# Performance work log

Hardware: AMD Instinct MI355X
Metric: run time of the kernel (lower is better)

Reference implementation:

```python
import jax, jax.numpy as jnp
import numpy as np

N = 50000      # nodes
E = 800000     # edges
D_IN = 128
D_H = 512
D_OUT = 256
G = 512        # graphs in batch
EPS_GIN = 0.0  # GINConv default eps
LRELU_SLOPE = 1.5


def setup_inputs() -> dict:
    key = jax.random.key(0)
    ks = jax.random.split(key, 16)
    x = jax.random.normal(ks[0], (N, D_IN), dtype=jnp.float32)
    edge_index = jax.random.randint(ks[1], (2, E), 0, N, dtype=jnp.int64)
    batch = jnp.sort(jax.random.randint(ks[2], (N,), 0, G, dtype=jnp.int64))
    def lin(k, fan_in, fan_out):
        bound = 1.0 / np.sqrt(fan_in)
        k1, k2 = jax.random.split(k)
        W = jax.random.uniform(k1, (fan_in, fan_out), jnp.float32, -bound, bound)
        b = jax.random.uniform(k2, (fan_out,), jnp.float32, -bound, bound)
        return W, b
    W1, b1 = lin(ks[3], D_IN, D_H)
    W2, b2 = lin(ks[4], D_H, D_H)
    W3, b3 = lin(ks[5], D_H, D_H)
    W4, b4 = lin(ks[6], D_H, D_H)
    Wl, bl = lin(ks[7], D_H, D_OUT)
    return {"x": x, "edge_index": edge_index, "batch": batch,
            "W1": W1, "b1": b1, "W2": W2, "b2": b2,
            "W3": W3, "b3": b3, "W4": W4, "b4": b4,
            "Wl": Wl, "bl": bl}


def reference(x, edge_index, batch, W1, b1, W2, b2, W3, b3, W4, b4, Wl, bl):
    # GIN aggregation: sum neighbor (source) features at each target node
    src, dst = edge_index[0], edge_index[1]
    agg = jax.ops.segment_sum(x[src], dst, num_segments=N)  # [N, D_IN]
    h = (1.0 + EPS_GIN) * x + agg
    # 4-layer MLP (Dropout inactive in eval; LeakyReLU negative_slope=1.5)
    h = h @ W1 + b1
    h = jnp.where(h > 0, h, LRELU_SLOPE * h)
    h = jax.nn.relu(h @ W2 + b2)
    h = jax.nn.relu(h @ W3 + b3)
    h = h @ W4 + b4                      # [N, D_H]
    # global mean pool over graphs
    sums = jax.ops.segment_sum(h, batch, num_segments=G)          # [G, D_H]
    cnt = jax.ops.segment_sum(jnp.ones((N, 1), h.dtype), batch, num_segments=G)
    pooled = sums / jnp.maximum(cnt, 1.0)
    out = pooled @ Wl + bl               # [G, D_OUT]
    # F.normalize(dim=1, eps=1e-12)
    nrm = jnp.linalg.norm(out, axis=1, keepdims=True)
    return out / jnp.maximum(nrm, 1e-12)
```

## Files before the change

### kernel.cpp

```cpp
#include <hip/hip_runtime.h>
#include <hip/hip_bf16.h>
#include <cstdint>
#include <cstddef>

#define N_NODES 50000
#define N_EDGES 800000
#define D_IN 128
#define D_H 512
#define D_OUT 256
#define N_GRAPHS 512

#define BM 128
#define BN 256
#define BK 32
#define NBLK ((N_NODES + 255) / 256)
#define CT_SW 264
#define N_MT 391
#define MT_PER_XCD 49

#define NBUCK 196
#define BCAP 6144
#define E_PER_BLK 4096

#define SCAT_BLKS 196
#define TR_BLKS 240
#define CVTX_BLKS ((N_NODES * D_IN / 2 + 64 + 255) / 256)
#define MID_BLKS (SCAT_BLKS + TR_BLKS + CVTX_BLKS)

#define WC_BLKS 64

#define PSLOTS 5

#define XQ_SCALE 4096.0f
#define XQ_INV (1.0f / 4096.0f)

typedef __bf16 v8bf __attribute__((ext_vector_type(8)));
typedef float v4f __attribute__((ext_vector_type(4)));
typedef int v4i __attribute__((ext_vector_type(4)));

__device__ __forceinline__ float bf2f(unsigned short b) {
  return __uint_as_float(((unsigned int)b) << 16);
}
__device__ __forceinline__ unsigned short f2bf(float f) {
  unsigned int u = __float_as_uint(f);
  u += 0x7FFFu + ((u >> 16) & 1u);
  return (unsigned short)(u >> 16);
}

__device__ __forceinline__ void gload_lds16(const void* g, void* l) {
  __builtin_amdgcn_global_load_lds(
      (const __attribute__((address_space(1))) void*)g,
      (__attribute__((address_space(3))) void*)l, 16, 0, 0);
}

__global__ __launch_bounds__(256) void k_prep(const void* __restrict__ x,
                                              const void* __restrict__ ei,
                                              const void* __restrict__ batch,
                                              int* __restrict__ gcur,
                                              int* __restrict__ flags) {
  __shared__ int cnt[3];
  int t = threadIdx.x;
  gcur[t] = 0;
  if (t < 3) cnt[t] = 0;
  __syncthreads();
  const unsigned short* xs = (const unsigned short*)x;
  int c0 = 0;
  for (int k = t; k < 4096; k += 256) {
    unsigned int e = (xs[k] >> 7) & 0xFFu;
    if (e >= 0x90u) c0++;
  }
  atomicAdd(&cnt[0], c0);
  const int* e32 = (const int*)ei;
  int c1 = 0;
  for (int k = t; k < 512; k += 256)
    if (e32[2 * k + 1] != 0) c1++;
  atomicAdd(&cnt[1], c1);
  const int* b32 = (const int*)batch;
  int c2 = 0;
  {
    int w = (N_NODES - 512) + 2 * t + 1;
    if (b32[w] != 0) c2++;
  }
  atomicAdd(&cnt[2], c2);
  __syncthreads();
  if (t == 0) {
    flags[0] = (cnt[0] > 16) ? 1 : 0;
    flags[1] = (cnt[1] == 0) ? 1 : 0;
    flags[2] = (cnt[2] == 0) ? 1 : 0;
  }
}

__global__ __launch_bounds__(256) void k_mid(
    const void* __restrict__ x, const int* __restrict__ ei,
    const int* __restrict__ flags,
    const void* W1, const void* W2, const void* W3, const void* W4,
    const void* Wl, unsigned short* W1T, unsigned short* W2T,
    unsigned short* W3T, unsigned short* W4T, unsigned short* WlT,
    int* __restrict__ gcur, unsigned int* __restrict__ pairs,
    unsigned int* __restrict__ xi, int ne) {
  __shared__ __align__(16) char mshm[20480];
  int bid = blockIdx.x;
  int t = threadIdx.x;

  if (bid < SCAT_BLKS) {
    int* hist = (int*)mshm;
    int* sstart = hist + 256;
    int* gbase = sstart + 256;
    int* sh = gbase + 256;
    unsigned int* lbuf = (unsigned int*)(mshm + 4096);
    int e0 = bid * E_PER_BLK;
    int nloc = ne - e0;
    if (nloc > E_PER_BLK) nloc = E_PER_BLK;
    hist[t] = 0;
    __syncthreads();
    bool fe64 = flags[1] != 0;
    unsigned int pk[16];
    short bk[16], rk[16];
#pragma unroll
    for (int it = 0; it < 16; ++it) {
      int li = it * 256 + t;
      bk[it] = -1;
      if (li < nloc) {
        size_t e = (size_t)e0 + li;
        int s = fe64 ? ei[2 * e] : ei[e];
        int d = fe64 ? ei[2 * ((size_t)ne + e)] : ei[(size_t)ne + e];
        int b = d >> 8;
        pk[it] = (unsigned int)(s & 0xFFFF) | ((unsigned int)(d & 255) << 16) |
                 ((unsigned int)b << 24);
        bk[it] = (short)b;
        rk[it] = (short)atomicAdd(&hist[b], 1);
      }
    }
    __syncthreads();
    int cnt = hist[t];
    sh[t] = cnt;
    __syncthreads();
    for (int o = 1; o < 256; o <<= 1) {
      int a = sh[t];
      int bb = (t >= o) ? sh[t - o] : 0;
      __syncthreads();
      sh[t] = a + bb;
      __syncthreads();
    }
    sstart[t] = sh[t] - cnt;
    gbase[t] = (cnt > 0) ? atomicAdd(&gcur[t], cnt) : 0;
    __syncthreads();
#pragma unroll
    for (int it = 0; it < 16; ++it)
      if (bk[it] >= 0) lbuf[sstart[bk[it]] + rk[it]] = pk[it];
    __syncthreads();
    for (int i = t; i < nloc; i += 256) {
      unsigned int v = lbuf[i];
      int b = v >> 24;
      int off = gbase[b] + (i - sstart[b]);
      if (off < BCAP) pairs[(size_t)b * BCAP + off] = v;
    }
    return;
  }

  if (bid < SCAT_BLKS + TR_BLKS) {
    typedef unsigned short row65[65];
    row65* tile = (row65*)mshm;
    int b2 = bid - SCAT_BLKS;
    const void* src;
    unsigned short* dst;
    int R, C, tb;
    if (b2 < 16)        { src = W1; dst = W1T; R = 128; C = 512; tb = b2; }
    else if (b2 < 80)   { src = W2; dst = W2T; R = 512; C = 512; tb = b2 - 16; }
    else if (b2 < 144)  { src = W3; dst = W3T; R = 512; C = 512; tb = b2 - 80; }
    else if (b2 < 208)  { src = W4; dst = W4T; R = 512; C = 512; tb = b2 - 144; }
    else                { src = Wl; dst = WlT; R = 512; C = 256; tb = b2 - 208; }
    int tpr = C >> 6;
    int r0 = (tb / tpr) << 6, c0 = (tb % tpr) << 6;
    bool f32 = flags[0] != 0;
#pragma unroll
    for (int k = 0; k < 16; ++k) {
      int idx = k * 256 + t;
      int r = idx >> 6, c = idx & 63;
      unsigned short v =
          f32 ? f2bf(((const float*)src)[(size_t)(r0 + r) * C + c0 + c])
              : ((const unsigned short*)src)[(size_t)(r0 + r) * C + c0 + c];
      tile[c][r] = v;
    }
    __syncthreads();
#pragma unroll
    for (int k = 0; k < 16; ++k) {
      int idx = k * 256 + t;
      int r = idx >> 6, c = idx & 63;
      dst[(size_t)(c0 + r) * R + r0 + c] = tile[r][c];
    }
    return;
  }

  int i = (bid - SCAT_BLKS - TR_BLKS) * 256 + t;
  if (i >= N_NODES * D_IN / 2) {
    if (i < N_NODES * D_IN / 2 + 64) xi[i] = 0;
    return;
  }
  float v0, v1;
  if (flags[0]) {
    const float* xf = (const float*)x + (size_t)i * 2;
    v0 = xf[0];
    v1 = xf[1];
  } else {
    unsigned int p = ((const unsigned int*)x)[i];
    v0 = __uint_as_float((p & 0xFFFFu) << 16);
    v1 = __uint_as_float(p & 0xFFFF0000u);
  }
  int q0 = __float2int_rn(fminf(fmaxf(v0, -7.99f), 7.99f) * XQ_SCALE);
  int q1 = __float2int_rn(fminf(fmaxf(v1, -7.99f), 7.99f) * XQ_SCALE);
  xi[i] = ((unsigned int)q0 & 0xFFFFu) | ((unsigned int)q1 << 16);
}

__global__ __launch_bounds__(256) void kb_sort(
    const unsigned int* __restrict__ pairs, const int* __restrict__ gcur,
    int* __restrict__ rowptr, unsigned short* __restrict__ elist,
    const unsigned short* __restrict__ W4T,
    const unsigned short* __restrict__ WlT,
    const void* __restrict__ b4, const void* __restrict__ bl,
    const int* __restrict__ flags,
    unsigned short* __restrict__ WcT, float* __restrict__ bc) {
  __shared__ int sh[256];
  __shared__ int cursor[256];
  __shared__ unsigned int lpair[BCAP];
  __shared__ unsigned short sorted[BCAP];
  int b = blockIdx.x, t = threadIdx.x;

  if (b >= NBUCK) {
    int wb = b - NBUCK;
    if (wb < WC_BLKS) {
      float (*wlt)[4] = (float(*)[4])lpair;
      int n0w = wb * 4;
      for (int e = t; e < 2048; e += 256) {
        int j = e >> 2, ns = e & 3;
        wlt[j][ns] = bf2f(WlT[(size_t)(n0w + ns) * 512 + j]);
      }
      __syncthreads();
      float a0[4] = {0.f, 0.f, 0.f, 0.f}, a1[4] = {0.f, 0.f, 0.f, 0.f};
      for (int j = 0; j < 512; ++j) {
        v4f wv = *(const v4f*)&wlt[j][0];
        float x0 = bf2f(W4T[(size_t)j * 512 + t]);
        float x1 = bf2f(W4T[(size_t)j * 512 + t + 256]);
#pragma unroll
        for (int q = 0; q < 4; ++q) {
          a0[q] += x0 * wv[q];
          a1[q] += x1 * wv[q];
        }
      }
#pragma unroll
      for (int q = 0; q < 4; ++q) {
        WcT[(size_t)(n0w + q) * 512 + t]       = f2bf(a0[q]);
        WcT[(size_t)(n0w + q) * 512 + t + 256] = f2bf(a1[q]);
      }
    } else {
      float* bsh = (float*)lpair;
      bool fmw = flags[0] != 0;
      for (int e = t; e < 512; e += 256)
        bsh[e] = fmw ? ((const float*)b4)[e]
                     : bf2f(((const unsigned short*)b4)[e]);
      __syncthreads();
      float a = fmw ? ((const float*)bl)[t]
                    : bf2f(((const unsigned short*)bl)[t]);
      for (int j = 0; j < 512; ++j)
        a += bsh[j] * bf2f(WlT[(size_t)t * 512 + j]);
      bc[t] = a;
    }
    return;
  }

  int c = (t < NBUCK) ? gcur[t] : 0;
  if (c > BCAP) c = BCAP;
  sh[t] = c;
  __syncthreads();
  for (int o = 1; o < 256; o <<= 1) {
    int a = sh[t];
    int v = (t >= o) ? sh[t - o] : 0;
    __syncthreads();
    sh[t] = a + v;
    __syncthreads();
  }
  int base = (b == 0) ? 0 : sh[b - 1];
  int cnt = sh[b] - base;
  cursor[t] = 0;
  __syncthreads();
  for (int i = t; i < cnt; i += 256) {
    unsigned int v = pairs[(size_t)b * BCAP + i];
    lpair[i] = v;
    atomicAdd(&cursor[(v >> 16) & 255], 1);
  }
  __syncthreads();
  int nc = cursor[t];
  sh[t] = nc;
  __syncthreads();
  for (int o = 1; o < 256; o <<= 1) {
    int a = sh[t];
    int v = (t >= o) ? sh[t - o] : 0;
    __syncthreads();
    sh[t] = a + v;
    __syncthreads();
  }
  int nstart = sh[t] - nc;
  cursor[t] = nstart;
  int node = b * 256 + t;
  if (node <= N_NODES) rowptr[node] = base + nstart;
  __syncthreads();
  for (int i = t; i < cnt; i += 256) {
    unsigned int v = lpair[i];
    int r = atomicAdd(&cursor[(v >> 16) & 255], 1);
    sorted[r] = (unsigned short)(v & 0xFFFFu);
  }
  __syncthreads();
  for (int i = t; i < cnt; i += 256)
    elist[base + i] = sorted[i];
}

__global__ __launch_bounds__(256) void k_gather(
    const unsigned int* __restrict__ xi, const int* __restrict__ rowptr,
    const unsigned short* __restrict__ elist, unsigned int* __restrict__ h0) {
  int node = blockIdx.x * 4 + (threadIdx.x >> 6);
  if (node >= N_NODES) return;
  int lane = threadIdx.x & 63;
  int l15 = lane & 15;
  int grp = lane >> 4;
  int s0 = rowptr[node], s1 = rowptr[node + 1];
  int a[8];
  {
    v4i self = (v4i){0, 0, 0, 0};
    if (lane < 16) self = *(const v4i*)(xi + (size_t)node * 64 + l15 * 4);
#pragma unroll
    for (int q = 0; q < 4; ++q) {
      a[2 * q]     = (int)(short)(self[q] & 0xFFFF);
      a[2 * q + 1] = self[q] >> 16;
    }
  }
  for (int j0 = s0; j0 < s1; j0 += 64) {
    int jj = j0 + lane;
    int cnt = s1 - j0;
    cnt = cnt < 64 ? cnt : 64;
    int ev = (jj < s1) ? (int)elist[jj] : N_NODES;
    for (int j = 0; j < cnt; j += 4) {
      int src = __shfl(ev, j + grp, 64);
      v4i p = *(const v4i*)(xi + (size_t)src * 64 + l15 * 4);
#pragma unroll
      for (int q = 0; q < 4; ++q) {
        a[2 * q]     += (int)(short)(p[q] & 0xFFFF);
        a[2 * q + 1] += p[q] >> 16;
      }
    }
  }
#pragma unroll
  for (int k = 0; k < 8; ++k) {
    a[k] += __shfl_xor(a[k], 16, 64);
    a[k] += __shfl_xor(a[k], 32, 64);
  }
  if (lane < 16) {
    v4i o;
#pragma unroll
    for (int q = 0; q < 4; ++q) {
      unsigned int lo = f2bf((float)a[2 * q] * XQ_INV);
      unsigned int hi = f2bf((float)a[2 * q + 1] * XQ_INV);
      o[q] = (int)(lo | (hi << 16));
    }
    *(v4i*)(h0 + (size_t)node * 64 + l15 * 4) = o;
  }
}

template <int ACT, int OUT, bool SWZ, bool FB = false>
__global__ __launch_bounds__(512, 4) void gemm_bt(
    const unsigned short* __restrict__ A,
    const unsigned short* __restrict__ BT,
    const void* __restrict__ bias, const int* __restrict__ flags,
    const int* __restrict__ batchp, void* __restrict__ Cout,
    int M, int K, int Nc) {
  __shared__ __align__(16) unsigned short smem[2][BM * BK + BN * BK];

  const int tid  = threadIdx.x;
  const int wave = tid >> 6;
  const int lane = tid & 63;
  const int quad = lane >> 4;
  const int l15  = lane & 15;
  int m0, n0;
  if (SWZ) {
    int xcd = blockIdx.x & 7;
    int l = blockIdx.x >> 3;
    int mt = xcd * MT_PER_XCD + (l >> 1);
    if (mt >= N_MT) return;
    m0 = mt * BM;
    n0 = (l & 1) * BN;
  } else {
    n0 = blockIdx.x * BN;
    m0 = blockIdx.y * BM;
  }
  const int wm = (wave >> 2) * 64;
  const int wn = (wave & 3) * 64;
  const bool fm = flags[0] != 0;

  v4f acc[4][4];
#pragma unroll
  for (int i = 0; i < 4; ++i)
#pragma unroll
    for (int j = 0; j < 4; ++j) acc[i][j] = (v4f){0.f, 0.f, 0.f, 0.f};

  auto stage = [&](int kt, int buf) {
    const int k0 = kt * BK;
    unsigned short* As = smem[buf];
    unsigned short* Bs = smem[buf] + BM * BK;
    {
      int L = tid;
      int row = L >> 2;
      int c = (L & 3) ^ ((row >> 1) & 3);
      int gr = m0 + row;
      gr = gr < M ? gr : (M - 1);
      gload_lds16(A + (size_t)gr * K + (k0 + c * 8), As + (size_t)L * 8);
    }
#pragma unroll
    for (int it = 0; it < 2; ++it) {
      int L = tid + it * 512;
      int row = L >> 2;
      int c = (L & 3) ^ ((row >> 1) & 3);
      int gn = n0 + row;
      gload_lds16(BT + (size_t)gn * K + (k0 + c * 8), Bs + (size_t)L * 8);
    }
  };

  const int nK = K / BK;
  stage(0, 0);
  for (int kt = 0; kt < nK; ++kt) {
    __syncthreads();
    if (kt + 1 < nK) stage(kt + 1, (kt + 1) & 1);
    const unsigned short* As = smem[kt & 1];
    const unsigned short* Bs = smem[kt & 1] + BM * BK;
    v8bf af[4], bfr[4];
#pragma unroll
    for (int mi = 0; mi < 4; ++mi) {
      int r = wm + mi * 16 + l15;
      int s = quad ^ ((r >> 1) & 3);
      af[mi] = *(const v8bf*)(As + (r * 4 + s) * 8);
    }
#pragma unroll
    for (int ni = 0; ni < 4; ++ni) {
      int r = wn + ni * 16 + l15;
      int s = quad ^ ((r >> 1) & 3);
      bfr[ni] = *(const v8bf*)(Bs + (r * 4 + s) * 8);
    }
#pragma unroll
    for (int mi = 0; mi < 4; ++mi)
#pragma unroll
      for (int ni = 0; ni < 4; ++ni)
        acc[mi][ni] = __builtin_amdgcn_mfma_f32_16x16x32_bf16(
            af[mi], bfr[ni], acc[mi][ni], 0, 0, 0);
  }

  float bv[4];
#pragma unroll
  for (int ni = 0; ni < 4; ++ni) {
    int col = n0 + wn + ni * 16 + l15;
    bv[ni] = (fm || FB) ? ((const float*)bias)[col]
                        : bf2f(((const unsigned short*)bias)[col]);
  }
#pragma unroll
  for (int mi = 0; mi < 4; ++mi)
#pragma unroll
    for (int ni = 0; ni < 4; ++ni)
#pragma unroll
      for (int rg = 0; rg < 4; ++rg) {
        float v = acc[mi][ni][rg] + bv[ni];
        if (ACT == 0) v = v > 0.f ? v : 1.5f * v;
        if (ACT == 1) v = v > 0.f ? v : 0.f;
        acc[mi][ni][rg] = v;
      }

  if (OUT == 1) {
#pragma unroll
    for (int ni = 0; ni < 4; ++ni) {
      int col = n0 + wn + ni * 16 + l15;
#pragma unroll
      for (int mi = 0; mi < 4; ++mi)
#pragma unroll
        for (int rg = 0; rg < 4; ++rg) {
          int row = m0 + wm + mi * 16 + quad * 4 + rg;
          if (row < M)
            ((float*)Cout)[(size_t)row * Nc + col] = acc[mi][ni][rg];
        }
    }
    return;
  }

  if (OUT == 2) {
    float* ssq = (float*)smem;
    __syncthreads();
    float pp[4][4];
#pragma unroll
    for (int mi = 0; mi < 4; ++mi)
#pragma unroll
      for (int rg = 0; rg < 4; ++rg) {
        float s = 0.f;
#pragma unroll
        for (int ni = 0; ni < 4; ++ni) {
          float v = acc[mi][ni][rg];
          s += v * v;
        }
#pragma unroll
        for (int o = 1; o < 16; o <<= 1) s += __shfl_xor(s, o, 64);
        pp[mi][rg] = s;
      }
    if (l15 == 0) {
#pragma unroll
      for (int mi = 0; mi < 4; ++mi)
#pragma unroll
        for (int rg = 0; rg < 4; ++rg)
          ssq[(wave & 3) * 128 + wm + mi * 16 + quad * 4 + rg] = pp[mi][rg];
    }
    __syncthreads();
#pragma unroll
    for (int mi = 0; mi < 4; ++mi)
#pragma unroll
      for (int rg = 0; rg < 4; ++rg) {
        int row = wm + mi * 16 + quad * 4 + rg;
        float tot = (ssq[row] + ssq[128 + row]) + (ssq[256 + row] + ssq[384 + row]);
        float inv = 1.0f / fmaxf(sqrtf(tot), 1e-12f);
        int grow = m0 + row;
#pragma unroll
        for (int ni = 0; ni < 4; ++ni) {
          int col = wn + ni * 16 + l15;
          float r = acc[mi][ni][rg] * inv;
          if (fm)
            ((float*)Cout)[(size_t)grow * Nc + col] = r;
          else
            ((unsigned short*)Cout)[(size_t)grow * Nc + col] = f2bf(r);
        }
      }
    return;
  }

  if (OUT == 3) {
    float* part = (float*)smem;
    __syncthreads();
    for (int i = tid; i < 8 * PSLOTS * 256; i += 512) part[i] = 0.f;
    const int contrib = (wave >> 2) * 4 + quad;
    const bool b64 = flags[2] != 0;
    int g0 = b64 ? batchp[2 * (size_t)m0] : batchp[m0];
    __syncthreads();
    int curslot = -1;
    float r0 = 0.f, r1 = 0.f, r2 = 0.f, r3 = 0.f;
#pragma unroll
    for (int mi = 0; mi < 4; ++mi)
#pragma unroll
      for (int rg = 0; rg < 4; ++rg) {
        int grow = m0 + wm + mi * 16 + quad * 4 + rg;
        if (grow < M) {
          int gv = (b64 ? batchp[2 * (size_t)grow] : batchp[grow]) - g0;
          gv = gv < 0 ? 0 : (gv >= PSLOTS ? PSLOTS - 1 : gv);
          if (gv != curslot) {
            if (curslot >= 0) {
              float* pp = part + (contrib * PSLOTS + curslot) * 256 + wn + l15;
              pp[0] += r0; pp[16] += r1; pp[32] += r2; pp[48] += r3;
            }
            curslot = gv;
            r0 = r1 = r2 = r3 = 0.f;
          }
          r0 += acc[mi][0][rg];
          r1 += acc[mi][1][rg];
          r2 += acc[mi][2][rg];
          r3 += acc[mi][3][rg];
        }
      }
    if (curslot >= 0) {
      float* pp = part + (contrib * PSLOTS + curslot) * 256 + wn + l15;
      pp[0] += r0; pp[16] += r1; pp[32] += r2; pp[48] += r3;
    }
    __syncthreads();
    float* pb = (float*)Cout;
    int mt = m0 >> 7;
    int nh = n0 >> 8;
    size_t base = (size_t)(mt * 2 + nh) * (PSLOTS * 256);
    for (int i = tid; i < PSLOTS * 256; i += 512) {
      float s = ((part[i] + part[1 * PSLOTS * 256 + i]) +
                 (part[2 * PSLOTS * 256 + i] + part[3 * PSLOTS * 256 + i])) +
                ((part[4 * PSLOTS * 256 + i] + part[5 * PSLOTS * 256 + i]) +
                 (part[6 * PSLOTS * 256 + i] + part[7 * PSLOTS * 256 + i]));
      pb[base + i] = s;
    }
    return;
  }

  unsigned short* Ct = (unsigned short*)smem;
  __syncthreads();
#pragma unroll
  for (int h = 0; h < 2; ++h) {
    if ((wave >> 2) == h) {
#pragma unroll
      for (int mi = 0; mi < 4; ++mi)
#pragma unroll
        for (int ni = 0; ni < 4; ++ni)
#pragma unroll
          for (int rg = 0; rg < 4; ++rg) {
            int lr = mi * 16 + quad * 4 + rg;
            int c = wn + ni * 16 + l15;
            Ct[lr * CT_SW + c] = f2bf(acc[mi][ni][rg]);
          }
    }
    __syncthreads();
    int rl0 = tid >> 5;
    int ch = tid & 31;
#pragma unroll
    for (int p = 0; p < 4; ++p) {
      int rl = rl0 + p * 16;
      int grow = m0 + h * 64 + rl;
      if (grow < M) {
        v4i val = *(const v4i*)(Ct + rl * CT_SW + ch * 8);
        *(v4i*)((unsigned short*)Cout + (size_t)grow * Nc + n0 + ch * 8) = val;
      }
    }
    __syncthreads();
  }
}

__global__ __launch_bounds__(256) void k_cvtpool(
    const float* __restrict__ pb, const int* __restrict__ batch,
    const int* __restrict__ flags, unsigned int* __restrict__ pooled) {
  __shared__ int bounds[2];
  int g = blockIdx.x, t = threadIdx.x;
  bool b64 = flags[2] != 0;
  if (t < 2) {
    int key = g + t;
    int lo = 0, hi = N_NODES;
    while (lo < hi) {
      int mid = (lo + hi) >> 1;
      int bv = b64 ? batch[2 * (size_t)mid] : batch[mid];
      if (bv < key) lo = mid + 1; else hi = mid;
    }
    bounds[t] = lo;
  }
  __syncthreads();
  int s0 = bounds[0], s1 = bounds[1];
  int c0 = 2 * t;
  int nh = c0 >> 8;
  int cl = c0 & 255;
  float a0 = 0.f, a1 = 0.f;
  if (s1 > s0) {
    int mtlo = s0 >> 7, mthi = (s1 - 1) >> 7;
    for (int mt = mtlo; mt <= mthi; ++mt) {
      int g0 = b64 ? batch[2 * (size_t)(mt * 128)] : batch[mt * 128];
      int slot = g - g0;
      if (slot >= 0 && slot < PSLOTS) {
        size_t base = (size_t)(mt * 2 + nh) * (PSLOTS * 256) + (size_t)slot * 256;
        a0 += pb[base + cl];
        a1 += pb[base + cl + 1];
      }
    }
  }
  float inv = 1.0f / fmaxf((float)(s1 - s0), 1.0f);
  unsigned int lo2 = f2bf(a0 * inv);
  unsigned int hi2 = f2bf(a1 * inv);
  pooled[(size_t)g * (D_H / 2) + t] = lo2 | (hi2 << 16);
}

extern "C" void kernel_launch(void* const* d_in, const int* in_sizes, int n_in,
                              void* d_out, int out_size, void* d_ws,
                              size_t ws_size, hipStream_t stream) {
  const void* x    = d_in[0];
  const int* ei    = (const int*)d_in[1];
  const int* batch = (const int*)d_in[2];
  const void* W1 = d_in[3];
  const void* b1 = d_in[4];
  const void* W2 = d_in[5];
  const void* b2 = d_in[6];
  const void* W3 = d_in[7];
  const void* b3 = d_in[8];
  const void* W4 = d_in[9];
  const void* b4 = d_in[10];
  const void* Wl = d_in[11];
  const void* bl = d_in[12];

  char* ws = (char*)d_ws;
  size_t off = 0;
  auto alloc = [&](size_t bytes) {
    void* p = ws + off;
    off += (bytes + 255) & ~(size_t)255;
    return p;
  };
  int* flags           = (int*)alloc(64);
  unsigned short* W1T  = (unsigned short*)alloc((size_t)D_IN * D_H * 2);
  unsigned short* W2T  = (unsigned short*)alloc((size_t)D_H * D_H * 2);
  unsigned short* W3T  = (unsigned short*)alloc((size_t)D_H * D_H * 2);
  unsigned short* W4T  = (unsigned short*)alloc((size_t)D_H * D_H * 2);
  unsigned short* WlT  = (unsigned short*)alloc((size_t)D_H * D_OUT * 2);
  unsigned short* WcT  = (unsigned short*)alloc((size_t)D_OUT * D_H * 2);
  float* bc            = (float*)alloc((size_t)D_OUT * 4);
  unsigned int* pooled3 = (unsigned int*)alloc((size_t)N_GRAPHS * D_H * 2);
  float* pb            = (float*)alloc((size_t)N_MT * 2 * PSLOTS * 256 * 4);
  int* gcur   = (int*)alloc(256 * 4);
  int* rowptr = (int*)alloc(((size_t)N_NODES + 1) * 4);
  unsigned short* elist = (unsigned short*)alloc((size_t)N_EDGES * 2);
  void* S1 = alloc((size_t)N_NODES * D_H * 2);
  void* S2 = alloc((size_t)N_NODES * D_H * 2);
  unsigned int* xi   = (unsigned int*)S1;
  unsigned short* hA = (unsigned short*)S1;
  unsigned int* pairs = (unsigned int*)((char*)S1 + ((size_t)16 << 20));
  unsigned int* h0u  = (unsigned int*)S2;
  unsigned short* h0 = (unsigned short*)S2;
  unsigned short* hB = (unsigned short*)S2;

  k_prep<<<1, 256, 0, stream>>>(x, ei, batch, gcur, flags);

  k_mid<<<MID_BLKS, 256, 0, stream>>>(
      x, ei, flags, W1, W2, W3, W4, Wl, W1T, W2T, W3T, W4T, WlT,
      gcur, pairs, xi, N_EDGES);

  kb_sort<<<NBUCK + WC_BLKS + 1, 256, 0, stream>>>(
      pairs, gcur, rowptr, elist, W4T, WlT, b4, bl, flags, WcT, bc);
  k_gather<<<(N_NODES + 3) / 4, 256, 0, stream>>>(xi, rowptr, elist, h0u);

  const int gBig = 8 * MT_PER_XCD * 2;
  gemm_bt<0, 0, true><<<gBig, 512, 0, stream>>>(
      h0, W1T, b1, flags, batch, hA, N_NODES, D_IN, D_H);
  gemm_bt<1, 0, true><<<gBig, 512, 0, stream>>>(
      hA, W2T, b2, flags, batch, hB, N_NODES, D_H, D_H);
  gemm_bt<1, 3, true><<<gBig, 512, 0, stream>>>(
      hB, W3T, b3, flags, batch, pb, N_NODES, D_H, D_H);

  k_cvtpool<<<N_GRAPHS, 256, 0, stream>>>(pb, batch, flags, pooled3);

  dim3 g5(1, 4);
  gemm_bt<2, 2, false, true><<<g5, 512, 0, stream>>>(
      (const unsigned short*)pooled3, WcT, bc, flags, batch, d_out,
      N_GRAPHS, D_H, D_OUT);
}
```

Measured before the change: 290.4 us.

## Fold format-detection prep kernel into k_mid and unroll gather loop by two

Removes the single-block k_prep launch by having every k_mid block recompute the dtype-detection counts it needs locally, with block 0 writing the flags for later kernels, and replaces gcur zeroing with a memset. This drops one serialized kernel launch and its dependency. Separately, the neighbor gather loop now issues two row loads per iteration to raise memory-level parallelism. Every k_mid block redundantly reads a few KB of input, and the 8-stride loop relies on padded elist entries pointing to a zeroed row.

```diff
diff --git a/kernel.cpp b/kernel.cpp
--- a/kernel.cpp
+++ b/kernel.cpp
@@ -53,56 +53,47 @@
       (__attribute__((address_space(3))) void*)l, 16, 0, 0);
 }
 
-__global__ __launch_bounds__(256) void k_prep(const void* __restrict__ x,
-                                              const void* __restrict__ ei,
-                                              const void* __restrict__ batch,
-                                              int* __restrict__ gcur,
-                                              int* __restrict__ flags) {
-  __shared__ int cnt[3];
-  int t = threadIdx.x;
-  gcur[t] = 0;
-  if (t < 3) cnt[t] = 0;
-  __syncthreads();
-  const unsigned short* xs = (const unsigned short*)x;
-  int c0 = 0;
-  for (int k = t; k < 4096; k += 256) {
-    unsigned int e = (xs[k] >> 7) & 0xFFu;
-    if (e >= 0x90u) c0++;
-  }
-  atomicAdd(&cnt[0], c0);
-  const int* e32 = (const int*)ei;
-  int c1 = 0;
-  for (int k = t; k < 512; k += 256)
-    if (e32[2 * k + 1] != 0) c1++;
-  atomicAdd(&cnt[1], c1);
-  const int* b32 = (const int*)batch;
-  int c2 = 0;
-  {
-    int w = (N_NODES - 512) + 2 * t + 1;
-    if (b32[w] != 0) c2++;
-  }
-  atomicAdd(&cnt[2], c2);
-  __syncthreads();
-  if (t == 0) {
-    flags[0] = (cnt[0] > 16) ? 1 : 0;
-    flags[1] = (cnt[1] == 0) ? 1 : 0;
-    flags[2] = (cnt[2] == 0) ? 1 : 0;
-  }
-}
-
 __global__ __launch_bounds__(256) void k_mid(
     const void* __restrict__ x, const int* __restrict__ ei,
-    const int* __restrict__ flags,
+    const void* __restrict__ batch, int* __restrict__ flagsOut,
     const void* W1, const void* W2, const void* W3, const void* W4,
     const void* Wl, unsigned short* W1T, unsigned short* W2T,
     unsigned short* W3T, unsigned short* W4T, unsigned short* WlT,
     int* __restrict__ gcur, unsigned int* __restrict__ pairs,
     unsigned int* __restrict__ xi, int ne) {
   __shared__ __align__(16) char mshm[20480];
+  __shared__ int fcnt[4];
   int bid = blockIdx.x;
   int t = threadIdx.x;
 
   if (bid < SCAT_BLKS) {
+    if (t < 4) fcnt[t] = 0;
+    __syncthreads();
+    const int* e32 = (const int*)ei;
+    int c1 = 0;
+    for (int k = t; k < 512; k += 256)
+      if (e32[2 * k + 1] != 0) c1++;
+    if (c1) atomicAdd(&fcnt[1], c1);
+    if (bid == 0) {
+      const unsigned short* xs = (const unsigned short*)x;
+      int c0 = 0;
+      for (int k = t; k < 4096; k += 256) {
+        unsigned int e = (xs[k] >> 7) & 0xFFu;
+        if (e >= 0x90u) c0++;
+      }
+      if (c0) atomicAdd(&fcnt[0], c0);
+      const int* b32 = (const int*)batch;
+      int w = (N_NODES - 512) + 2 * t + 1;
+      if (b32[w] != 0) atomicAdd(&fcnt[2], 1);
+    }
+    __syncthreads();
+    bool fe64 = (fcnt[1] == 0);
+    if (bid == 0 && t == 0) {
+      flagsOut[0] = (fcnt[0] > 16) ? 1 : 0;
+      flagsOut[1] = (fcnt[1] == 0) ? 1 : 0;
+      flagsOut[2] = (fcnt[2] == 0) ? 1 : 0;
+    }
+
     int* hist = (int*)mshm;
     int* sstart = hist + 256;
     int* gbase = sstart + 256;
@@ -113,7 +104,6 @@
     if (nloc > E_PER_BLK) nloc = E_PER_BLK;
     hist[t] = 0;
     __syncthreads();
-    bool fe64 = flags[1] != 0;
     unsigned int pk[16];
     short bk[16], rk[16];
 #pragma unroll
@@ -157,6 +147,20 @@
     }
     return;
   }
+
+  if (t == 0) fcnt[0] = 0;
+  __syncthreads();
+  {
+    const unsigned short* xs = (const unsigned short*)x;
+    int c0 = 0;
+    for (int k = t; k < 4096; k += 256) {
+      unsigned int e = (xs[k] >> 7) & 0xFFu;
+      if (e >= 0x90u) c0++;
+    }
+    if (c0) atomicAdd(&fcnt[0], c0);
+  }
+  __syncthreads();
+  bool f32 = fcnt[0] > 16;
 
   if (bid < SCAT_BLKS + TR_BLKS) {
     typedef unsigned short row65[65];
@@ -172,7 +176,6 @@
     else                { src = Wl; dst = WlT; R = 512; C = 256; tb = b2 - 208; }
     int tpr = C >> 6;
     int r0 = (tb / tpr) << 6, c0 = (tb % tpr) << 6;
-    bool f32 = flags[0] != 0;
 #pragma unroll
     for (int k = 0; k < 16; ++k) {
       int idx = k * 256 + t;
@@ -198,7 +201,7 @@
     return;
   }
   float v0, v1;
-  if (flags[0]) {
+  if (f32) {
     const float* xf = (const float*)x + (size_t)i * 2;
     v0 = xf[0];
     v1 = xf[1];
@@ -338,13 +341,20 @@
     int cnt = s1 - j0;
     cnt = cnt < 64 ? cnt : 64;
     int ev = (jj < s1) ? (int)elist[jj] : N_NODES;
-    for (int j = 0; j < cnt; j += 4) {
-      int src = __shfl(ev, j + grp, 64);
-      v4i p = *(const v4i*)(xi + (size_t)src * 64 + l15 * 4);
+    for (int j = 0; j < cnt; j += 8) {
+      int sa = __shfl(ev, j + grp, 64);
+      int sb = __shfl(ev, j + 4 + grp, 64);
+      v4i p0 = *(const v4i*)(xi + (size_t)sa * 64 + l15 * 4);
+      v4i p1 = *(const v4i*)(xi + (size_t)sb * 64 + l15 * 4);
 #pragma unroll
       for (int q = 0; q < 4; ++q) {
-        a[2 * q]     += (int)(short)(p[q] & 0xFFFF);
-        a[2 * q + 1] += p[q] >> 16;
+        a[2 * q]     += (int)(short)(p0[q] & 0xFFFF);
+        a[2 * q + 1] += p0[q] >> 16;
+      }
+#pragma unroll
+      for (int q = 0; q < 4; ++q) {
+        a[2 * q]     += (int)(short)(p1[q] & 0xFFFF);
+        a[2 * q + 1] += p1[q] >> 16;
       }
     }
   }
@@ -702,10 +712,10 @@
   unsigned short* h0 = (unsigned short*)S2;
   unsigned short* hB = (unsigned short*)S2;
 
-  k_prep<<<1, 256, 0, stream>>>(x, ei, batch, gcur, flags);
+  hipMemsetAsync(gcur, 0, 256 * 4, stream);
 
   k_mid<<<MID_BLKS, 256, 0, stream>>>(
-      x, ei, flags, W1, W2, W3, W4, Wl, W1T, W2T, W3T, W4T, WlT,
+      x, ei, batch, flags, W1, W2, W3, W4, Wl, W1T, W2T, W3T, W4T, WlT,
       gcur, pairs, xi, N_EDGES);
 
   kb_sort<<<NBUCK + WC_BLKS + 1, 256, 0, stream>>>(
```

New measurement: 301.0 us. 3.6% more time.
